# Kernel optimization log

Measured on AMD Instinct MI355X. Metric: run time of the kernel, lower is better.

Reference implementation:

```python
import jax, jax.numpy as jnp
import numpy as np

B, N, L, M, F = 32, 32, 512, 64, 64
EPS = 1e-8

def setup_inputs() -> dict:
    key = jax.random.key(0)
    k1, k2, k3, k4, k5 = jax.random.split(key, 5)
    x_aug = jax.random.normal(k1, (B, N, L, F), dtype=jnp.float32)
    # monotone time grid in [0,1], shape (L,1) so it broadcasts against (1,N,1,M)
    t = jnp.linspace(0.0, 1.0, L, dtype=jnp.float32)[:, None]
    t_left = jax.random.uniform(k2, (N, M), dtype=jnp.float32) * 0.8
    t_right = t_left + 0.05 + 0.15 * jax.random.uniform(k3, (N, M), dtype=jnp.float32)
    kappa = jax.random.normal(k4, (N, 1), dtype=jnp.float32)
    return {"x_aug": x_aug, "t": t, "t_left": t_left, "t_right": t_right, "kappa": kappa}

def reference(x_aug, t, t_left, t_right, kappa):
    # kappa: (N,1) -> softplus -> (1,N,1,1)
    k = jax.nn.softplus(kappa)[None, :, None]          # (1,N,1,1)
    tl = t_left[None, :, None, :]                       # (1,N,1,M)
    tr = t_right[None, :, None, :]                      # (1,N,1,M)
    # soft box kernel over time: alpha (1,N,L,M)
    alpha = jax.nn.sigmoid((tr - t) / k) * jax.nn.sigmoid((t - tl) / k)
    # weighted pool over L without materializing (B,N,L,M,F)
    numerator = jnp.einsum('bnlf,nlm->bnmf', x_aug, alpha[0])  # (B,N,M,F)
    denominator = alpha.sum(axis=2)[..., None]                 # (1,N,M,1)
    return numerator / (denominator + EPS)
```

## Files before the change

### kernel.cpp

```cpp
#include <hip/hip_runtime.h>
#include <math.h>

typedef unsigned short u16;
typedef unsigned int   u32;
typedef __attribute__((ext_vector_type(8))) short short8;
typedef __attribute__((ext_vector_type(4))) float f32x4;

namespace {
constexpr int Bb = 32, Nn = 32, Ll = 512, Mm = 64, Ff = 64;
constexpr int TL  = 32;
constexpr int NT  = Ll / TL;
constexpr int TLP = 40;
constexpr float EPSV = 1e-8f;
constexpr size_t AW_ELEMS = (size_t)Nn * Ll * Mm;
constexpr size_t AW_BYTES = AW_ELEMS * 2 * 2;
}

__device__ __forceinline__ u16 bf16rne(float x) {
    u32 u = __float_as_uint(x);
    return (u16)((u + 0x7fffu + ((u >> 16) & 1u)) >> 16);
}
__device__ __forceinline__ float bf16tof(u16 h) {
    return __uint_as_float(((u32)h) << 16);
}

__global__ __launch_bounds__(256)
void alpha_kernel(const float* __restrict__ t_in,
                  const float* __restrict__ t_left,
                  const float* __restrict__ t_right,
                  const float* __restrict__ kappa,
                  u16* __restrict__ awh, u16* __restrict__ awl)
{
    const int n   = blockIdx.x;
    const int tid = threadIdx.x;

    __shared__ float ts[Ll];
    __shared__ float dred[4][Mm];
    __shared__ float inv[Mm];

    for (int i = tid; i < Ll; i += 256) ts[i] = t_in[i];

    const float kap = kappa[n];
    const float kk  = fmaxf(kap, 0.0f) + log1pf(expf(-fabsf(kap)));
    const float ik  = 1.0f / kk;

    const int m1 = tid & 63, lq = tid >> 6;
    const float tl1 = t_left[n * Mm + m1], tr1 = t_right[n * Mm + m1];
    __syncthreads();
    float ds = 0.0f;
    for (int l = lq; l < Ll; l += 4) {
        const float tv = ts[l];
        ds += 1.0f / ((1.0f + __expf((tv - tr1) * ik)) *
                      (1.0f + __expf((tl1 - tv) * ik)));
    }
    dred[lq][m1] = ds;
    __syncthreads();
    if (tid < Mm)
        inv[tid] = 1.0f / (dred[0][tid] + dred[1][tid] + dred[2][tid] + dred[3][tid] + EPSV);
    __syncthreads();

    const int mm = tid >> 2, seg = tid & 3;
    const float tl2 = t_left[n * Mm + mm], tr2 = t_right[n * Mm + mm];
    const float iv = inv[mm];
    for (int l = seg * 128; l < seg * 128 + 128; l += 2) {
        float tv = ts[l];
        const float v0 = iv / ((1.0f + __expf((tv - tr2) * ik)) *
                               (1.0f + __expf((tl2 - tv) * ik)));
        tv = ts[l + 1];
        const float v1 = iv / ((1.0f + __expf((tv - tr2) * ik)) *
                               (1.0f + __expf((tl2 - tv) * ik)));
        const u16 h0 = bf16rne(v0), h1 = bf16rne(v1);
        const u16 s0 = bf16rne(v0 - bf16tof(h0)), s1 = bf16rne(v1 - bf16tof(h1));
        const size_t idx = ((size_t)(n * NT + (l >> 5)) * Mm + mm) * TL + (l & 31);
        *(u32*)&awh[idx] = (u32)h0 | ((u32)h1 << 16);
        *(u32*)&awl[idx] = (u32)s0 | ((u32)s1 << 16);
    }
}

__global__ __launch_bounds__(256, 2)
void wagg_mfma(const float* __restrict__ x_aug,
               const u16* __restrict__ awh, const u16* __restrict__ awl,
               float* __restrict__ out)
{
    const int n   = blockIdx.x & 31;
    const int b0  = (blockIdx.x >> 5) * 2;
    const int tid = threadIdx.x;

    __shared__ u16 ah_s[2][Mm * TLP];
    __shared__ u16 al_s[2][Mm * TLP];
    __shared__ u16 xh_s[2][2 * Ff * TLP];
    __shared__ u16 xl_s[2][2 * Ff * TLP];

    const int fq = tid & 15;
    const int lp = tid >> 4;
    const int am = tid & 63;
    const int aq = tid >> 6;

    const float* xb[2] = {
        x_aug + (size_t)(b0 * Nn + n) * (Ll * Ff),
        x_aug + (size_t)((b0 + 1) * Nn + n) * (Ll * Ff)
    };
    const u16* ahg = awh + (size_t)n * NT * Mm * TL;
    const u16* alg = awl + (size_t)n * NT * Mm * TL;

    const int lane = tid & 63;
    const int w    = tid >> 6;
    const int bw   = w & 1;
    const int mg   = w >> 1;
    const int q    = lane >> 4;
    const int c    = lane & 15;

    f32x4 acc[2][4];
    #pragma unroll
    for (int mi = 0; mi < 2; ++mi)
        #pragma unroll
        for (int ft = 0; ft < 4; ++ft)
            acc[mi][ft] = (f32x4){0.f, 0.f, 0.f, 0.f};

    float X[2][2][4];
    uint4 AH, AL;

    {
        #pragma unroll
        for (int bi = 0; bi < 2; ++bi) {
            const float* p = xb[bi] + (size_t)(2 * lp) * Ff + fq * 4;
            *(float4*)X[bi][0] = *(const float4*)p;
            *(float4*)X[bi][1] = *(const float4*)(p + Ff);
        }
        AH = *(const uint4*)(ahg + (size_t)am * TL + aq * 8);
        AL = *(const uint4*)(alg + (size_t)am * TL + aq * 8);

        #pragma unroll
        for (int bi = 0; bi < 2; ++bi)
            #pragma unroll
            for (int j = 0; j < 4; ++j) {
                const float v0 = X[bi][0][j], v1 = X[bi][1][j];
                const u16 h0 = bf16rne(v0), h1 = bf16rne(v1);
                const u16 s0 = bf16rne(v0 - bf16tof(h0)), s1 = bf16rne(v1 - bf16tof(h1));
                const u32 off = (u32)(bi * Ff + fq * 4 + j) * TLP + 2 * lp;
                *(u32*)&xh_s[0][off] = (u32)h0 | ((u32)h1 << 16);
                *(u32*)&xl_s[0][off] = (u32)s0 | ((u32)s1 << 16);
            }
        *(uint4*)&ah_s[0][am * TLP + aq * 8] = AH;
        *(uint4*)&al_s[0][am * TLP + aq * 8] = AL;
    }
    __syncthreads();

    for (int tile = 0; tile < NT; ++tile) {
        const int cur = tile & 1, nxt = cur ^ 1;

        if (tile + 1 < NT) {
            const int l0 = (tile + 1) * TL;
            #pragma unroll
            for (int bi = 0; bi < 2; ++bi) {
                const float* p = xb[bi] + (size_t)(l0 + 2 * lp) * Ff + fq * 4;
                *(float4*)X[bi][0] = *(const float4*)p;
                *(float4*)X[bi][1] = *(const float4*)(p + Ff);
            }
            const size_t ao = (size_t)(tile + 1) * Mm * TL + am * TL + aq * 8;
            AH = *(const uint4*)(ahg + ao);
            AL = *(const uint4*)(alg + ao);
        }

        short8 ahf[2], alf[2], xhf[4], xlf[4];
        #pragma unroll
        for (int mi = 0; mi < 2; ++mi) {
            const u32 off = (u32)((mg * 2 + mi) * 16 + c) * TLP + q * 8;
            ahf[mi] = *(const short8*)&ah_s[cur][off];
            alf[mi] = *(const short8*)&al_s[cur][off];
        }
        #pragma unroll
        for (int ft = 0; ft < 4; ++ft) {
            const u32 off = (u32)(bw * Ff + ft * 16 + c) * TLP + q * 8;
            xhf[ft] = *(const short8*)&xh_s[cur][off];
            xlf[ft] = *(const short8*)&xl_s[cur][off];
        }
        #pragma unroll
        for (int mi = 0; mi < 2; ++mi)
            #pragma unroll
            for (int ft = 0; ft < 4; ++ft) {
                acc[mi][ft] = __builtin_amdgcn_mfma_f32_16x16x32_bf16(
                    ahf[mi], xhf[ft], acc[mi][ft], 0, 0, 0);
                acc[mi][ft] = __builtin_amdgcn_mfma_f32_16x16x32_bf16(
                    ahf[mi], xlf[ft], acc[mi][ft], 0, 0, 0);
                acc[mi][ft] = __builtin_amdgcn_mfma_f32_16x16x32_bf16(
                    alf[mi], xhf[ft], acc[mi][ft], 0, 0, 0);
            }

        if (tile + 1 < NT) {
            #pragma unroll
            for (int bi = 0; bi < 2; ++bi)
                #pragma unroll
                for (int j = 0; j < 4; ++j) {
                    const float v0 = X[bi][0][j], v1 = X[bi][1][j];
                    const u16 h0 = bf16rne(v0), h1 = bf16rne(v1);
                    const u16 s0 = bf16rne(v0 - bf16tof(h0)), s1 = bf16rne(v1 - bf16tof(h1));
                    const u32 off = (u32)(bi * Ff + fq * 4 + j) * TLP + 2 * lp;
                    *(u32*)&xh_s[nxt][off] = (u32)h0 | ((u32)h1 << 16);
                    *(u32*)&xl_s[nxt][off] = (u32)s0 | ((u32)s1 << 16);
                }
            *(uint4*)&ah_s[nxt][am * TLP + aq * 8] = AH;
            *(uint4*)&al_s[nxt][am * TLP + aq * 8] = AL;
        }
        __syncthreads();
    }

    float* ob = out + (size_t)((b0 + bw) * Nn + n) * (Mm * Ff);
    #pragma unroll
    for (int mi = 0; mi < 2; ++mi) {
        const int mbase = (mg * 2 + mi) * 16 + q * 4;
        #pragma unroll
        for (int r = 0; r < 4; ++r)
            #pragma unroll
            for (int ft = 0; ft < 4; ++ft)
                ob[(size_t)(mbase + r) * Ff + ft * 16 + c] = acc[mi][ft][r];
    }
}

__global__ __launch_bounds__(256, 1)
void wagg_fallback(const float* __restrict__ x_aug,
                   const float* __restrict__ t_in,
                   const float* __restrict__ t_left,
                   const float* __restrict__ t_right,
                   const float* __restrict__ kappa,
                   float* __restrict__ out)
{
    constexpr int BG = 4;
    const int n   = blockIdx.x >> 3;
    const int b0  = (blockIdx.x & 7) * BG;
    const int tid = threadIdx.x;

    __shared__ float xs[BG][TL][Ff];
    __shared__ float as_[TL][Mm];
    __shared__ float ts[Ll];
    __shared__ float dred[4][Mm];

    for (int i = tid; i < Ll; i += 256) ts[i] = t_in[i];

    const int am  = tid & 63;
    const int alq = tid >> 6;
    const float kap = kappa[n];
    const float kk  = fmaxf(kap, 0.0f) + log1pf(expf(-fabsf(kap)));
    const float ik  = 1.0f / kk;
    const float tlv = t_left [n * Mm + am];
    const float trv = t_right[n * Mm + am];

    const int bs   = tid >> 6;
    const int lane = tid & 63;
    const int mi   = (lane >> 3) << 3;
    const int fi   = (lane & 7) << 3;

    float acc[8][8];
    #pragma unroll
    for (int i = 0; i < 8; ++i)
        #pragma unroll
        for (int j = 0; j < 8; ++j) acc[i][j] = 0.0f;

    float4 stg[8];
    float  aval[8];
    float  dpart = 0.0f;

    __syncthreads();
    {
        #pragma unroll
        for (int k = 0; k < 8; ++k) {
            const int g = k * 256 + tid;
            const int gbs = g >> 9, r = (g >> 4) & 31, fqq = (g & 15) << 2;
            stg[k] = *(const float4*)(x_aug
                + (size_t)((b0 + gbs) * Nn + n) * (Ll * Ff) + (size_t)r * Ff + fqq);
        }
        #pragma unroll
        for (int i = 0; i < 8; ++i) {
            const float tv = ts[alq + (i << 2)];
            const float a = 1.0f / ((1.0f + __expf((tv - trv) * ik)) *
                                    (1.0f + __expf((tlv - tv) * ik)));
            aval[i] = a; dpart += a;
        }
        #pragma unroll
        for (int k = 0; k < 8; ++k) ((float4*)xs)[k * 256 + tid] = stg[k];
        #pragma unroll
        for (int i = 0; i < 8; ++i) as_[alq + (i << 2)][am] = aval[i];
    }
    __syncthreads();

    for (int tile = 0; tile < NT; ++tile) {
        if (tile + 1 < NT) {
            const int l0 = (tile + 1) * TL;
            #pragma unroll
            for (int k = 0; k < 8; ++k) {
                const int g = k * 256 + tid;
                const int gbs = g >> 9, r = (g >> 4) & 31, fqq = (g & 15) << 2;
                stg[k] = *(const float4*)(x_aug
                    + (size_t)((b0 + gbs) * Nn + n) * (Ll * Ff)
                    + (size_t)(l0 + r) * Ff + fqq);
            }
            #pragma unroll
            for (int i = 0; i < 8; ++i) {
                const float tv = ts[l0 + alq + (i << 2)];
                const float a = 1.0f / ((1.0f + __expf((tv - trv) * ik)) *
                                        (1.0f + __expf((tlv - tv) * ik)));
                aval[i] = a; dpart += a;
            }
        }
        #pragma unroll 4
        for (int lt = 0; lt < TL; ++lt) {
            float av[8], xv[8];
            *(float4*)&av[0] = *(const float4*)&as_[lt][mi];
            *(float4*)&av[4] = *(const float4*)&as_[lt][mi + 4];
            *(float4*)&xv[0] = *(const float4*)&xs[bs][lt][fi];
            *(float4*)&xv[4] = *(const float4*)&xs[bs][lt][fi + 4];
            #pragma unroll
            for (int i = 0; i < 8; ++i)
                #pragma unroll
                for (int j = 0; j < 8; ++j)
                    acc[i][j] = fmaf(av[i], xv[j], acc[i][j]);
        }
        __syncthreads();
        if (tile + 1 < NT) {
            #pragma unroll
            for (int k = 0; k < 8; ++k) ((float4*)xs)[k * 256 + tid] = stg[k];
            #pragma unroll
            for (int i = 0; i < 8; ++i) as_[alq + (i << 2)][am] = aval[i];
        }
        __syncthreads();
    }

    dred[alq][am] = dpart;
    __syncthreads();
    if (tid < Mm) {
        const float d = dred[0][tid] + dred[1][tid] + dred[2][tid] + dred[3][tid];
        dred[0][tid] = 1.0f / (d + EPSV);
    }
    __syncthreads();

    const size_t obase = ((size_t)(b0 + bs) * Nn + n) * Mm;
    #pragma unroll
    for (int i = 0; i < 8; ++i) {
        const float inv = dred[0][mi + i];
        float o[8];
        #pragma unroll
        for (int j = 0; j < 8; ++j) o[j] = acc[i][j] * inv;
        float* dst = out + (obase + (mi + i)) * Ff + fi;
        *(float4*)dst       = *(float4*)&o[0];
        *((float4*)dst + 1) = *(float4*)&o[4];
    }
}

extern "C" void kernel_launch(void* const* d_in, const int* in_sizes, int n_in,
                              void* d_out, int out_size, void* d_ws, size_t ws_size,
                              hipStream_t stream)
{
    const float* x_aug   = (const float*)d_in[0];
    const float* t_in    = (const float*)d_in[1];
    const float* t_left  = (const float*)d_in[2];
    const float* t_right = (const float*)d_in[3];
    const float* kappa   = (const float*)d_in[4];
    float* out = (float*)d_out;

    if (ws_size >= AW_BYTES) {
        u16* awh = (u16*)d_ws;
        u16* awl = awh + AW_ELEMS;
        hipLaunchKernelGGL(alpha_kernel, dim3(Nn), dim3(256), 0, stream,
                           t_in, t_left, t_right, kappa, awh, awl);
        hipLaunchKernelGGL(wagg_mfma, dim3((Bb / 2) * Nn), dim3(256), 0, stream,
                           x_aug, awh, awl, out);
    } else {
        hipLaunchKernelGGL(wagg_fallback, dim3(Nn * 8), dim3(256), 0, stream,
                           x_aug, t_in, t_left, t_right, kappa, out);
    }
}
```

Baseline: 236.3 us.

## Split denominator into separate kernel, widen alpha grid, one batch per MFMA block

The alpha computation is split into a denominator kernel and an alpha-weight kernel, each launched over 256 blocks instead of 32, so that more CUs share the preprocessing work. The MFMA aggregation kernel now handles one batch per block (1024 blocks) with smaller LDS, and its launch bounds are raised to 4 blocks per SM for higher occupancy. The cost is an extra kernel launch, and each weight tile is now reloaded from global memory by twice as many blocks.

```diff
diff --git a/kernel.cpp b/kernel.cpp
--- a/kernel.cpp
+++ b/kernel.cpp
@@ -12,8 +12,9 @@
 constexpr int NT  = Ll / TL;
 constexpr int TLP = 40;
 constexpr float EPSV = 1e-8f;
-constexpr size_t AW_ELEMS = (size_t)Nn * Ll * Mm;
-constexpr size_t AW_BYTES = AW_ELEMS * 2 * 2;
+constexpr size_t DEN_ELEMS = (size_t)Nn * Mm;
+constexpr size_t AW_ELEMS  = (size_t)Nn * Ll * Mm;
+constexpr size_t WS_BYTES  = DEN_ELEMS * 4 + AW_ELEMS * 2 * 2;
 }
 
 __device__ __forceinline__ u16 bf16rne(float x) {
@@ -22,6 +23,49 @@
 }
 __device__ __forceinline__ float bf16tof(u16 h) {
     return __uint_as_float(((u32)h) << 16);
+}
+
+__global__ __launch_bounds__(256)
+void denom_kernel(const float* __restrict__ t_in,
+                  const float* __restrict__ t_left,
+                  const float* __restrict__ t_right,
+                  const float* __restrict__ kappa,
+                  float* __restrict__ denom)
+{
+    const int n  = blockIdx.x >> 3;
+    const int mg = blockIdx.x & 7;
+    const int tid = threadIdx.x;
+    const int m8 = tid & 7;
+    const int lq = tid >> 3;
+
+    __shared__ float ts[Ll];
+    __shared__ float red[32][8];
+
+    for (int i = tid; i < Ll; i += 256) ts[i] = t_in[i];
+
+    const int m = mg * 8 + m8;
+    const float kap = kappa[n];
+    const float kk  = fmaxf(kap, 0.0f) + log1pf(expf(-fabsf(kap)));
+    const float ik  = 1.0f / kk;
+    const float tlv = t_left [n * Mm + m];
+    const float trv = t_right[n * Mm + m];
+    __syncthreads();
+
+    float s = 0.0f;
+    #pragma unroll
+    for (int i = 0; i < 16; ++i) {
+        const float tv = ts[lq + i * 32];
+        s += 1.0f / ((1.0f + __expf((tv - trv) * ik)) *
+                     (1.0f + __expf((tlv - tv) * ik)));
+    }
+    red[lq][m8] = s;
+    __syncthreads();
+    if (tid < 8) {
+        float d = 0.0f;
+        #pragma unroll
+        for (int i = 0; i < 32; ++i) d += red[i][tid];
+        denom[n * Mm + mg * 8 + tid] = d;
+    }
 }
 
 __global__ __launch_bounds__(256)
@@ -29,118 +73,95 @@
                   const float* __restrict__ t_left,
                   const float* __restrict__ t_right,
                   const float* __restrict__ kappa,
+                  const float* __restrict__ denom,
                   u16* __restrict__ awh, u16* __restrict__ awl)
 {
-    const int n   = blockIdx.x;
+    const int n  = blockIdx.x >> 3;
+    const int ls = blockIdx.x & 7;
     const int tid = threadIdx.x;
-
-    __shared__ float ts[Ll];
-    __shared__ float dred[4][Mm];
-    __shared__ float inv[Mm];
-
-    for (int i = tid; i < Ll; i += 256) ts[i] = t_in[i];
+    const int m  = tid & 63;
+    const int li = tid >> 6;
+
+    __shared__ float ts2[64];
+    if (tid < 64) ts2[tid] = t_in[ls * 64 + tid];
 
     const float kap = kappa[n];
     const float kk  = fmaxf(kap, 0.0f) + log1pf(expf(-fabsf(kap)));
     const float ik  = 1.0f / kk;
-
-    const int m1 = tid & 63, lq = tid >> 6;
-    const float tl1 = t_left[n * Mm + m1], tr1 = t_right[n * Mm + m1];
-    __syncthreads();
-    float ds = 0.0f;
-    for (int l = lq; l < Ll; l += 4) {
-        const float tv = ts[l];
-        ds += 1.0f / ((1.0f + __expf((tv - tr1) * ik)) *
-                      (1.0f + __expf((tl1 - tv) * ik)));
-    }
-    dred[lq][m1] = ds;
-    __syncthreads();
-    if (tid < Mm)
-        inv[tid] = 1.0f / (dred[0][tid] + dred[1][tid] + dred[2][tid] + dred[3][tid] + EPSV);
-    __syncthreads();
-
-    const int mm = tid >> 2, seg = tid & 3;
-    const float tl2 = t_left[n * Mm + mm], tr2 = t_right[n * Mm + mm];
-    const float iv = inv[mm];
-    for (int l = seg * 128; l < seg * 128 + 128; l += 2) {
-        float tv = ts[l];
-        const float v0 = iv / ((1.0f + __expf((tv - tr2) * ik)) *
-                               (1.0f + __expf((tl2 - tv) * ik)));
-        tv = ts[l + 1];
-        const float v1 = iv / ((1.0f + __expf((tv - tr2) * ik)) *
-                               (1.0f + __expf((tl2 - tv) * ik)));
+    const float tlv = t_left [n * Mm + m];
+    const float trv = t_right[n * Mm + m];
+    const float iv  = 1.0f / (denom[n * Mm + m] + EPSV);
+    __syncthreads();
+
+    #pragma unroll
+    for (int j = 0; j < 16; j += 2) {
+        const int ll = li * 16 + j;
+        const int l  = ls * 64 + ll;
+        float tv = ts2[ll];
+        const float v0 = iv / ((1.0f + __expf((tv - trv) * ik)) *
+                               (1.0f + __expf((tlv - tv) * ik)));
+        tv = ts2[ll + 1];
+        const float v1 = iv / ((1.0f + __expf((tv - trv) * ik)) *
+                               (1.0f + __expf((tlv - tv) * ik)));
         const u16 h0 = bf16rne(v0), h1 = bf16rne(v1);
         const u16 s0 = bf16rne(v0 - bf16tof(h0)), s1 = bf16rne(v1 - bf16tof(h1));
-        const size_t idx = ((size_t)(n * NT + (l >> 5)) * Mm + mm) * TL + (l & 31);
+        const size_t idx = ((size_t)(n * NT + (l >> 5)) * Mm + m) * TL + (l & 31);
         *(u32*)&awh[idx] = (u32)h0 | ((u32)h1 << 16);
         *(u32*)&awl[idx] = (u32)s0 | ((u32)s1 << 16);
     }
 }
 
-__global__ __launch_bounds__(256, 2)
+__global__ __launch_bounds__(256, 4)
 void wagg_mfma(const float* __restrict__ x_aug,
                const u16* __restrict__ awh, const u16* __restrict__ awl,
                float* __restrict__ out)
 {
-    const int n   = blockIdx.x & 31;
-    const int b0  = (blockIdx.x >> 5) * 2;
+    const int n   = blockIdx.x >> 5;
+    const int b   = blockIdx.x & 31;
     const int tid = threadIdx.x;
 
     __shared__ u16 ah_s[2][Mm * TLP];
     __shared__ u16 al_s[2][Mm * TLP];
-    __shared__ u16 xh_s[2][2 * Ff * TLP];
-    __shared__ u16 xl_s[2][2 * Ff * TLP];
+    __shared__ u16 xh_s[2][Ff * TLP];
+    __shared__ u16 xl_s[2][Ff * TLP];
 
     const int fq = tid & 15;
     const int lp = tid >> 4;
     const int am = tid & 63;
     const int aq = tid >> 6;
 
-    const float* xb[2] = {
-        x_aug + (size_t)(b0 * Nn + n) * (Ll * Ff),
-        x_aug + (size_t)((b0 + 1) * Nn + n) * (Ll * Ff)
-    };
+    const float* xb = x_aug + (size_t)(b * Nn + n) * (Ll * Ff);
     const u16* ahg = awh + (size_t)n * NT * Mm * TL;
     const u16* alg = awl + (size_t)n * NT * Mm * TL;
 
     const int lane = tid & 63;
     const int w    = tid >> 6;
-    const int bw   = w & 1;
-    const int mg   = w >> 1;
     const int q    = lane >> 4;
     const int c    = lane & 15;
 
-    f32x4 acc[2][4];
-    #pragma unroll
-    for (int mi = 0; mi < 2; ++mi)
-        #pragma unroll
-        for (int ft = 0; ft < 4; ++ft)
-            acc[mi][ft] = (f32x4){0.f, 0.f, 0.f, 0.f};
-
-    float X[2][2][4];
+    f32x4 acc[4];
+    #pragma unroll
+    for (int ft = 0; ft < 4; ++ft) acc[ft] = (f32x4){0.f, 0.f, 0.f, 0.f};
+
+    float X[2][4];
     uint4 AH, AL;
 
     {
-        #pragma unroll
-        for (int bi = 0; bi < 2; ++bi) {
-            const float* p = xb[bi] + (size_t)(2 * lp) * Ff + fq * 4;
-            *(float4*)X[bi][0] = *(const float4*)p;
-            *(float4*)X[bi][1] = *(const float4*)(p + Ff);
-        }
+        const float* p = xb + (size_t)(2 * lp) * Ff + fq * 4;
+        *(float4*)X[0] = *(const float4*)p;
+        *(float4*)X[1] = *(const float4*)(p + Ff);
         AH = *(const uint4*)(ahg + (size_t)am * TL + aq * 8);
         AL = *(const uint4*)(alg + (size_t)am * TL + aq * 8);
 
         #pragma unroll
-        for (int bi = 0; bi < 2; ++bi)
-            #pragma unroll
-            for (int j = 0; j < 4; ++j) {
-                const float v0 = X[bi][0][j], v1 = X[bi][1][j];
-                const u16 h0 = bf16rne(v0), h1 = bf16rne(v1);
-                const u16 s0 = bf16rne(v0 - bf16tof(h0)), s1 = bf16rne(v1 - bf16tof(h1));
-                const u32 off = (u32)(bi * Ff + fq * 4 + j) * TLP + 2 * lp;
-                *(u32*)&xh_s[0][off] = (u32)h0 | ((u32)h1 << 16);
-                *(u32*)&xl_s[0][off] = (u32)s0 | ((u32)s1 << 16);
-            }
+        for (int j = 0; j < 4; ++j) {
+            const float v0 = X[0][j], v1 = X[1][j];
+            const u16 h0 = bf16rne(v0), h1 = bf16rne(v1);
+            const u16 s0 = bf16rne(v0 - bf16tof(h0)), s1 = bf16rne(v1 - bf16tof(h1));
+            const u32 off = (u32)(fq * 4 + j) * TLP + 2 * lp;
+            *(u32*)&xh_s[0][off] = (u32)h0 | ((u32)h1 << 16);
+            *(u32*)&xl_s[0][off] = (u32)s0 | ((u32)s1 << 16);
+        }
         *(uint4*)&ah_s[0][am * TLP + aq * 8] = AH;
         *(uint4*)&al_s[0][am * TLP + aq * 8] = AL;
     }
@@ -150,71 +171,56 @@
         const int cur = tile & 1, nxt = cur ^ 1;
 
         if (tile + 1 < NT) {
-            const int l0 = (tile + 1) * TL;
-            #pragma unroll
-            for (int bi = 0; bi < 2; ++bi) {
-                const float* p = xb[bi] + (size_t)(l0 + 2 * lp) * Ff + fq * 4;
-                *(float4*)X[bi][0] = *(const float4*)p;
-                *(float4*)X[bi][1] = *(const float4*)(p + Ff);
-            }
+            const float* p = xb + (size_t)((tile + 1) * TL + 2 * lp) * Ff + fq * 4;
+            *(float4*)X[0] = *(const float4*)p;
+            *(float4*)X[1] = *(const float4*)(p + Ff);
             const size_t ao = (size_t)(tile + 1) * Mm * TL + am * TL + aq * 8;
             AH = *(const uint4*)(ahg + ao);
             AL = *(const uint4*)(alg + ao);
         }
 
-        short8 ahf[2], alf[2], xhf[4], xlf[4];
-        #pragma unroll
-        for (int mi = 0; mi < 2; ++mi) {
-            const u32 off = (u32)((mg * 2 + mi) * 16 + c) * TLP + q * 8;
-            ahf[mi] = *(const short8*)&ah_s[cur][off];
-            alf[mi] = *(const short8*)&al_s[cur][off];
+        short8 ahf, alf, xhf[4], xlf[4];
+        {
+            const u32 off = (u32)(w * 16 + c) * TLP + q * 8;
+            ahf = *(const short8*)&ah_s[cur][off];
+            alf = *(const short8*)&al_s[cur][off];
         }
         #pragma unroll
         for (int ft = 0; ft < 4; ++ft) {
-            const u32 off = (u32)(bw * Ff + ft * 16 + c) * TLP + q * 8;
+            const u32 off = (u32)(ft * 16 + c) * TLP + q * 8;
             xhf[ft] = *(const short8*)&xh_s[cur][off];
             xlf[ft] = *(const short8*)&xl_s[cur][off];
         }
         #pragma unroll
-        for (int mi = 0; mi < 2; ++mi)
-            #pragma unroll
-            for (int ft = 0; ft < 4; ++ft) {
-                acc[mi][ft] = __builtin_amdgcn_mfma_f32_16x16x32_bf16(
-                    ahf[mi], xhf[ft], acc[mi][ft], 0, 0, 0);
-                acc[mi][ft] = __builtin_amdgcn_mfma_f32_16x16x32_bf16(
-                    ahf[mi], xlf[ft], acc[mi][ft], 0, 0, 0);
-                acc[mi][ft] = __builtin_amdgcn_mfma_f32_16x16x32_bf16(
-                    alf[mi], xhf[ft], acc[mi][ft], 0, 0, 0);
+        for (int ft = 0; ft < 4; ++ft) {
+            acc[ft] = __builtin_amdgcn_mfma_f32_16x16x32_bf16(ahf, xhf[ft], acc[ft], 0, 0, 0);
+            acc[ft] = __builtin_amdgcn_mfma_f32_16x16x32_bf16(ahf, xlf[ft], acc[ft], 0, 0, 0);
+            acc[ft] = __builtin_amdgcn_mfma_f32_16x16x32_bf16(alf, xhf[ft], acc[ft], 0, 0, 0);
+        }
+
+        if (tile + 1 < NT) {
+            #pragma unroll
+            for (int j = 0; j < 4; ++j) {
+                const float v0 = X[0][j], v1 = X[1][j];
+                const u16 h0 = bf16rne(v0), h1 = bf16rne(v1);
+                const u16 s0 = bf16rne(v0 - bf16tof(h0)), s1 = bf16rne(v1 - bf16tof(h1));
+                const u32 off = (u32)(fq * 4 + j) * TLP + 2 * lp;
+                *(u32*)&xh_s[nxt][off] = (u32)h0 | ((u32)h1 << 16);
+                *(u32*)&xl_s[nxt][off] = (u32)s0 | ((u32)s1 << 16);
             }
-
-        if (tile + 1 < NT) {
-            #pragma unroll
-            for (int bi = 0; bi < 2; ++bi)
-                #pragma unroll
-                for (int j = 0; j < 4; ++j) {
-                    const float v0 = X[bi][0][j], v1 = X[bi][1][j];
-                    const u16 h0 = bf16rne(v0), h1 = bf16rne(v1);
-                    const u16 s0 = bf16rne(v0 - bf16tof(h0)), s1 = bf16rne(v1 - bf16tof(h1));
-                    const u32 off = (u32)(bi * Ff + fq * 4 + j) * TLP + 2 * lp;
-                    *(u32*)&xh_s[nxt][off] = (u32)h0 | ((u32)h1 << 16);
-                    *(u32*)&xl_s[nxt][off] = (u32)s0 | ((u32)s1 << 16);
-                }
             *(uint4*)&ah_s[nxt][am * TLP + aq * 8] = AH;
             *(uint4*)&al_s[nxt][am * TLP + aq * 8] = AL;
         }
         __syncthreads();
     }
 
-    float* ob = out + (size_t)((b0 + bw) * Nn + n) * (Mm * Ff);
-    #pragma unroll
-    for (int mi = 0; mi < 2; ++mi) {
-        const int mbase = (mg * 2 + mi) * 16 + q * 4;
-        #pragma unroll
-        for (int r = 0; r < 4; ++r)
-            #pragma unroll
-            for (int ft = 0; ft < 4; ++ft)
-                ob[(size_t)(mbase + r) * Ff + ft * 16 + c] = acc[mi][ft][r];
-    }
+    float* ob = out + (size_t)(b * Nn + n) * (Mm * Ff);
+    const int mbase = w * 16 + q * 4;
+    #pragma unroll
+    for (int r = 0; r < 4; ++r)
+        #pragma unroll
+        for (int ft = 0; ft < 4; ++ft)
+            ob[(size_t)(mbase + r) * Ff + ft * 16 + c] = acc[ft][r];
 }
 
 __global__ __launch_bounds__(256, 1)
@@ -357,12 +363,15 @@
     const float* kappa   = (const float*)d_in[4];
     float* out = (float*)d_out;
 
-    if (ws_size >= AW_BYTES) {
-        u16* awh = (u16*)d_ws;
+    if (ws_size >= WS_BYTES) {
+        float* denom = (float*)d_ws;
+        u16* awh = (u16*)(denom + DEN_ELEMS);
         u16* awl = awh + AW_ELEMS;
-        hipLaunchKernelGGL(alpha_kernel, dim3(Nn), dim3(256), 0, stream,
-                           t_in, t_left, t_right, kappa, awh, awl);
-        hipLaunchKernelGGL(wagg_mfma, dim3((Bb / 2) * Nn), dim3(256), 0, stream,
+        hipLaunchKernelGGL(denom_kernel, dim3(Nn * 8), dim3(256), 0, stream,
+                           t_in, t_left, t_right, kappa, denom);
+        hipLaunchKernelGGL(alpha_kernel, dim3(Nn * 8), dim3(256), 0, stream,
+                           t_in, t_left, t_right, kappa, denom, awh, awl);
+        hipLaunchKernelGGL(wagg_mfma, dim3(Nn * Bb), dim3(256), 0, stream,
                            x_aug, awh, awl, out);
     } else {
         hipLaunchKernelGGL(wagg_fallback, dim3(Nn * 8), dim3(256), 0, stream,
```

Measured after the change: 218.5 us. -7.5%, faster.
